# Kernel optimization log

Hardware: AMD Instinct MI355X
Metric: run time of the kernel (lower is better)

The kernel has to match this reference:

```python
import jax, jax.numpy as jnp
import numpy as np
from jax import lax

# Sizes
B, N, F = 8, 4096, 64          # clouds, points per cloud, feature dim
RATIO, RADIUS, K = 0.5, 0.2, 64  # fps ratio, ball radius, max_num_neighbors
S = int(N * RATIO)              # sampled centroids per cloud
H1, H2, H3 = 64, 64, 128        # MLP widths


def setup_inputs() -> dict:
    key = jax.random.key(0)
    ks = jax.random.split(key, 6)
    x = jax.random.normal(ks[0], (B * N, F), jnp.float32)
    pos = jax.random.uniform(ks[1], (B * N, 3), jnp.float32)  # unit cube
    batch = (jnp.arange(B * N) // N).astype(jnp.int32)  # equal-size clouds
    W1 = jax.random.normal(ks[2], (F + 3, H1), jnp.float32) * 0.1
    b1 = jnp.zeros((H1,), jnp.float32)
    W2 = jax.random.normal(ks[3], (H1, H2), jnp.float32) * 0.1
    b2 = jnp.zeros((H2,), jnp.float32)
    W3 = jax.random.normal(ks[4], (H2, H3), jnp.float32) * 0.1
    b3 = jnp.zeros((H3,), jnp.float32)
    return dict(x=x, pos=pos, batch=batch, W1=W1, b1=b1, W2=W2, b2=b2, W3=W3, b3=b3)


def fps_indices(pos_b):
    """Farthest point sampling for one cloud. pos_b: [N,3] -> [S] int32 indices."""
    def step(carry, _):
        cur, dmin = carry
        d = jnp.sum((pos_b - pos_b[cur]) ** 2, axis=-1)  # [N]
        dmin = jnp.minimum(dmin, d)
        nxt = jnp.argmax(dmin).astype(jnp.int32)
        return (nxt, dmin), cur
    init = (jnp.int32(0), jnp.full((N,), jnp.inf, jnp.float32))
    (_, _), sel = lax.scan(step, init, None, length=S)
    return sel


def reference(x, pos, batch, W1, b1, W2, b2, W3, b3):
    x3 = x.reshape(B, N, F)
    pos3 = pos.reshape(B, N, 3)
    batch3 = batch.reshape(B, N)

    # fps returns indices only -> no gradient path through sampling
    idx = jax.vmap(fps_indices)(lax.stop_gradient(pos3))  # [B,S]
    bi = jnp.arange(B)[:, None]
    pos_s = pos3[bi, idx]  # [B,S,3] sampled centroids

    # radius ball query: nearest-K within RADIUS (cap = max_num_neighbors)
    d2 = jnp.sum((pos_s[:, :, None, :] - pos3[:, None, :, :]) ** 2, axis=-1)  # [B,S,N]
    neg_d2, nbr = lax.top_k(-d2, K)          # [B,S,K] nearest K per centroid
    valid = (-neg_d2) <= RADIUS * RADIUS     # [B,S,K] inside-ball mask

    # PointNetConv: message = MLP(concat(x_j, pos_j - pos_i)), aggr = max
    gi = jnp.arange(B)[:, None, None]
    x_j = x3[gi, nbr]                          # [B,S,K,F]
    rel = pos3[gi, nbr] - pos_s[:, :, None, :]  # [B,S,K,3]
    h = jnp.concatenate([x_j, rel], axis=-1)    # [B,S,K,F+3]
    h = jax.nn.relu(h @ W1 + b1)
    h = jax.nn.relu(h @ W2 + b2)
    h = jax.nn.relu(h @ W3 + b3)                # [B,S,K,H3]
    h = jnp.where(valid[..., None], h, -jnp.inf)
    # each centroid is its own neighbor (dist 0 <= RADIUS), so max is finite
    out = jnp.max(h, axis=2)                    # [B,S,H3]

    x_out = out.reshape(B * S, H3)
    pos_out = pos_s.reshape(B * S, 3)
    batch_out = batch3[bi, idx].reshape(B * S)
    return x_out, pos_out, batch_out
```

## Files before the change

kernel.cpp:

```cpp
#include <hip/hip_runtime.h>
#include <cstdint>
#include <cstddef>

#define BB 8
#define NN 4096
#define FF 64
#define SS 2048
#define KK 64
#define H1c 64
#define H2c 64
#define H3c 128
#define R2 0.04f
#define CAP 448
#define NY1 240

typedef unsigned long long ull;
typedef __attribute__((ext_vector_type(4))) float f32x4;
typedef __attribute__((ext_vector_type(8))) short bf16x8;

__device__ __forceinline__ float d2_exact(float ax, float ay, float az,
                                          float bx, float by, float bz) {
  float dx = __fsub_rn(ax, bx);
  float dy = __fsub_rn(ay, by);
  float dz = __fsub_rn(az, bz);
  return __fadd_rn(__fadd_rn(__fmul_rn(dx, dx), __fmul_rn(dy, dy)), __fmul_rn(dz, dz));
}

__device__ __forceinline__ unsigned short f2bf(float f) {
  unsigned u = __float_as_uint(f);
  return (unsigned short)((u + 0x7fffu + ((u >> 16) & 1u)) >> 16);
}

#define WAVE_MAX_DPP(v)                                                        \
  do {                                                                         \
    v = max(v, __builtin_amdgcn_update_dpp(0, v, 0x111, 0xf, 0xf, true));      \
    v = max(v, __builtin_amdgcn_update_dpp(0, v, 0x112, 0xf, 0xf, true));      \
    v = max(v, __builtin_amdgcn_update_dpp(0, v, 0x114, 0xf, 0xf, true));      \
    v = max(v, __builtin_amdgcn_update_dpp(0, v, 0x118, 0xf, 0xf, true));      \
    v = max(v, __builtin_amdgcn_update_dpp(0, v, 0x142, 0xf, 0xf, true));      \
    v = max(v, __builtin_amdgcn_update_dpp(0, v, 0x143, 0xf, 0xf, true));      \
  } while (0)

__global__ __launch_bounds__(512) void fused_kernel(
    const float* __restrict__ pos, const float* __restrict__ x,
    const float* __restrict__ W1, const float* __restrict__ b1,
    const float* __restrict__ W2, const float* __restrict__ W3,
    float* __restrict__ pos_out, float* __restrict__ batch_out,
    unsigned short* __restrict__ y1b, unsigned short* __restrict__ w2p,
    unsigned short* __restrict__ w3p) {
  __shared__ __align__(16) char smem[49152];
  __shared__ ull skey[2][8];
  const int tid = threadIdx.x;

  if (blockIdx.x < BB) {
    float* plds = (float*)smem;
    const int b = blockIdx.x;
    const float4* src = (const float4*)(pos + (size_t)b * NN * 3);
    float4* dstl = (float4*)plds;
#pragma unroll
    for (int k = 0; k < 6; ++k) dstl[tid + k * 512] = src[tid + k * 512];
    __syncthreads();

    float px[8], py[8], pz[8], dmin[8];
#pragma unroll
    for (int i = 0; i < 8; ++i) {
      int p = tid * 8 + i;
      px[i] = plds[p * 3 + 0];
      py[i] = plds[p * 3 + 1];
      pz[i] = plds[p * 3 + 2];
      dmin[i] = INFINITY;
    }
    const int lane = tid & 63, wv = tid >> 6;
    float cx = plds[0], cy = plds[1], cz = plds[2];

    for (int s = 0; s < SS; ++s) {
      if (tid == 0) {
        int o = b * SS + s;
        pos_out[o * 3 + 0] = cx;
        pos_out[o * 3 + 1] = cy;
        pos_out[o * 3 + 2] = cz;
      }
#pragma unroll
      for (int i = 0; i < 8; ++i) {
        float d = d2_exact(px[i], py[i], pz[i], cx, cy, cz);
        dmin[i] = fminf(dmin[i], d);
      }
      float m0 = fmaxf(fmaxf(dmin[0], dmin[1]), fmaxf(dmin[2], dmin[3]));
      float m1 = fmaxf(fmaxf(dmin[4], dmin[5]), fmaxf(dmin[6], dmin[7]));
      const float lmax = fmaxf(m0, m1);
      int lidx = 0;
#pragma unroll
      for (int i = 7; i >= 0; --i)
        if (__float_as_int(dmin[i]) == __float_as_int(lmax)) lidx = i;

      const int lv = __float_as_int(lmax);
      int v = lv;
      WAVE_MAX_DPP(v);
      const int wmax = __builtin_amdgcn_readlane(v, 63);
      const ull bal = __ballot(lv == wmax);
      const int wl = (int)__builtin_ctzll(bal);
      const int wli = __builtin_amdgcn_readlane(lidx, wl);
      const int widx = ((wv << 6) + wl) * 8 + wli;
      const int buf = s & 1;
      if (lane == 0)
        skey[buf][wv] = ((ull)(unsigned)wmax << 32) | (unsigned)(~widx);
      __syncthreads();

      ull ka = skey[buf][0];
#pragma unroll
      for (int q = 1; q < 8; ++q) {
        ull kq = skey[buf][q];
        if (kq > ka) ka = kq;
      }
      const int cur = (int)(~(unsigned)(ka & 0xffffffffu));
      cx = plds[cur * 3 + 0];
      cy = plds[cur * 3 + 1];
      cz = plds[cur * 3 + 2];
    }
    for (int i = tid; i < SS; i += 512) batch_out[b * SS + i] = (float)b;
    return;
  }

  if (blockIdx.x == BB) {
    for (int e = tid; e < 4096; e += 512) {
      int j = e & 7, l = (e >> 3) & 63, s = (e >> 9) & 1, c = e >> 10;
      w2p[e] = f2bf(W2[(s * 32 + 8 * (l >> 4) + j) * H2c + c * 16 + (l & 15)]);
    }
    for (int e = tid; e < 8192; e += 512) {
      int j = e & 7, l = (e >> 3) & 63, s = (e >> 9) & 1, c = e >> 10;
      w3p[e] = f2bf(W3[(s * 32 + 8 * (l >> 4) + j) * H3c + c * 16 + (l & 15)]);
    }
    return;
  }

  float(*xs)[65] = (float(*)[65])smem;
  const int cid = blockIdx.x - BB - 1;
  for (int t = cid; t < 512; t += NY1) {
    const int r0 = t * 64;
    const float4* src = (const float4*)(x + (size_t)r0 * FF);
#pragma unroll
    for (int q = 0; q < 2; q++) {
      int p = tid + q * 512;
      float4 v = src[p];
      int row = (p * 4) >> 6, col = (p * 4) & 63;
      xs[row][col + 0] = v.x;
      xs[row][col + 1] = v.y;
      xs[row][col + 2] = v.z;
      xs[row][col + 3] = v.w;
    }
    __syncthreads();
    const int c4 = (tid & 15) * 4, kb = (tid >> 4) * 2;
    float acc[2][4];
#pragma unroll
    for (int kq = 0; kq < 2; kq++) {
      acc[kq][0] = b1[c4 + 0];
      acc[kq][1] = b1[c4 + 1];
      acc[kq][2] = b1[c4 + 2];
      acc[kq][3] = b1[c4 + 3];
    }
    for (int f = 0; f < FF; ++f) {
      float4 w = *(const float4*)(W1 + f * H1c + c4);
#pragma unroll
      for (int kq = 0; kq < 2; kq++) {
        float a = xs[kb + kq][f];
        acc[kq][0] += a * w.x;
        acc[kq][1] += a * w.y;
        acc[kq][2] += a * w.z;
        acc[kq][3] += a * w.w;
      }
    }
#pragma unroll
    for (int kq = 0; kq < 2; kq++) {
      ushort4 o;
      o.x = f2bf(acc[kq][0]);
      o.y = f2bf(acc[kq][1]);
      o.z = f2bf(acc[kq][2]);
      o.w = f2bf(acc[kq][3]);
      *(ushort4*)(y1b + (size_t)(r0 + kb + kq) * H1c + c4) = o;
    }
    __syncthreads();
  }
}

__global__ __launch_bounds__(256) void ballq_kernel(const float* __restrict__ pos,
                                                    const float* __restrict__ pos_out,
                                                    int* __restrict__ nbr) {
  __shared__ float plds[NN * 3];
  __shared__ __align__(16) ull kc[4][CAP];
  const int tid = threadIdx.x;
  const int b = blockIdx.x >> 6;
  const int chunk = blockIdx.x & 63;
  const float4* src = (const float4*)(pos + (size_t)b * NN * 3);
  float4* dstl = (float4*)plds;
#pragma unroll
  for (int k = 0; k < 12; k++) dstl[tid + k * 256] = src[tid + k * 256];
  __syncthreads();

  const int w = tid >> 6, lane = tid & 63;
  for (int t8 = 0; t8 < 8; ++t8) {
    const int s = chunk * 32 + w * 8 + t8;
    const int g = b * SS + s;
    const float cx = pos_out[g * 3 + 0], cy = pos_out[g * 3 + 1], cz = pos_out[g * 3 + 2];
    int cnt = 0;
    for (int t = 0; t < 64; ++t) {
      int j = t * 64 + lane;
      float d2 = d2_exact(plds[j * 3 + 0], plds[j * 3 + 1], plds[j * 3 + 2], cx, cy, cz);
      bool pred = (d2 <= R2);
      unsigned long long mask = __ballot(pred);
      if (pred) {
        int p = cnt + __popcll(mask & ((1ull << lane) - 1ull));
        if (p < CAP) kc[w][p] = ((ull)__float_as_uint(d2) << 32) | (unsigned)j;
      }
      cnt += (int)__popcll(mask);
    }
    int M = cnt < CAP ? cnt : CAP;
    __syncthreads();

    if (M <= 64) {
      int v = (lane < M) ? (b * NN + (int)(unsigned)(kc[w][lane] & 0xffffffffu)) : -1;
      nbr[(size_t)g * KK + lane] = v;
    } else {
      ull mk[7];
      int rk[7];
#pragma unroll
      for (int q = 0; q < 7; q++) {
        int p = lane + q * 64;
        mk[q] = (p < M) ? kc[w][p] : ~0ull;
        rk[q] = 0;
      }
      int i = 0;
      for (; i + 2 <= M; i += 2) {
        ull ka = kc[w][i], kb2 = kc[w][i + 1];
#pragma unroll
        for (int q = 0; q < 7; q++)
          rk[q] += (int)(ka < mk[q]) + (int)(kb2 < mk[q]);
      }
      if (i < M) {
        ull ka = kc[w][i];
#pragma unroll
        for (int q = 0; q < 7; q++) rk[q] += (int)(ka < mk[q]);
      }
#pragma unroll
      for (int q = 0; q < 7; q++) {
        int p = lane + q * 64;
        if (p < M && rk[q] < KK)
          nbr[(size_t)g * KK + rk[q]] = b * NN + (int)(unsigned)(mk[q] & 0xffffffffu);
      }
    }
    __syncthreads();
  }
}

__global__ __launch_bounds__(256) void mlp_kernel(
    const float* __restrict__ pos, const unsigned short* __restrict__ y1b,
    const float* __restrict__ W1, const float* __restrict__ b2,
    const float* __restrict__ b3, const unsigned short* __restrict__ w2p,
    const unsigned short* __restrict__ w3p, const int* __restrict__ nbr,
    const float* __restrict__ pos_out, float* __restrict__ x_out) {
  __shared__ __align__(16) unsigned short lw2[4096];
  __shared__ __align__(16) unsigned short lw3[8192];
  __shared__ float w1r[3][64];
  __shared__ int nl[64];
  __shared__ float red[4][128];
  __shared__ __align__(16) unsigned short h2t[4][16][88];
  const int tid = threadIdx.x;
  const int lane = tid & 63, wv = tid >> 6;
  const int lrow = lane & 15, g16 = lane >> 4;

  {
    const uint4* s2 = (const uint4*)w2p;
    uint4* d2v = (uint4*)lw2;
    for (int i = tid; i < 512; i += 256) d2v[i] = s2[i];
    const uint4* s3 = (const uint4*)w3p;
    uint4* d3v = (uint4*)lw3;
    for (int i = tid; i < 1024; i += 256) d3v[i] = s3[i];
    if (tid < 192) w1r[tid / 64][tid % 64] = W1[(64 + tid / 64) * H1c + (tid % 64)];
  }
  const bf16x8* w2f = (const bf16x8*)lw2;
  const bf16x8* w3f = (const bf16x8*)lw3;

  for (int pass = 0; pass < 4; ++pass) {
    const int g = blockIdx.x * 4 + pass;
    if (tid < 64) nl[tid] = nbr[(size_t)g * KK + tid];
    const float cx = pos_out[g * 3 + 0], cy = pos_out[g * 3 + 1],
                cz = pos_out[g * 3 + 2];
    __syncthreads();

    const int r = wv * 16 + lrow;
    const int j = nl[r];

    bf16x8 a0 = (bf16x8)0, a1 = (bf16x8)0;
    if (j >= 0) {
      const float rx = pos[j * 3 + 0] - cx;
      const float ry = pos[j * 3 + 1] - cy;
      const float rz = pos[j * 3 + 2] - cz;
      const unsigned short* yr = y1b + (size_t)j * H1c;
      uint4 vlo = *(const uint4*)(yr + 8 * g16);
      uint4 vhi = *(const uint4*)(yr + 32 + 8 * g16);
      const unsigned* plo = (const unsigned*)&vlo;
      const unsigned* phi = (const unsigned*)&vhi;
#pragma unroll
      for (int q = 0; q < 4; ++q) {
        unsigned u = plo[q];
        int k0 = 8 * g16 + 2 * q;
        float e0 = __uint_as_float(u << 16) + rx * w1r[0][k0] + ry * w1r[1][k0] +
                   rz * w1r[2][k0];
        float e1 = __uint_as_float(u & 0xffff0000u) + rx * w1r[0][k0 + 1] +
                   ry * w1r[1][k0 + 1] + rz * w1r[2][k0 + 1];
        a0[2 * q] = (short)f2bf(fmaxf(e0, 0.f));
        a0[2 * q + 1] = (short)f2bf(fmaxf(e1, 0.f));
        unsigned u2 = phi[q];
        int k1 = 32 + k0;
        float f0 = __uint_as_float(u2 << 16) + rx * w1r[0][k1] + ry * w1r[1][k1] +
                   rz * w1r[2][k1];
        float f1 = __uint_as_float(u2 & 0xffff0000u) + rx * w1r[0][k1 + 1] +
                   ry * w1r[1][k1 + 1] + rz * w1r[2][k1 + 1];
        a1[2 * q] = (short)f2bf(fmaxf(f0, 0.f));
        a1[2 * q + 1] = (short)f2bf(fmaxf(f1, 0.f));
      }
    }

#pragma unroll
    for (int c = 0; c < 4; ++c) {
      float bb = b2[c * 16 + lrow];
      f32x4 acc = {bb, bb, bb, bb};
      acc = __builtin_amdgcn_mfma_f32_16x16x32_bf16(a0, w2f[(c * 2 + 0) * 64 + lane], acc, 0, 0, 0);
      acc = __builtin_amdgcn_mfma_f32_16x16x32_bf16(a1, w2f[(c * 2 + 1) * 64 + lane], acc, 0, 0, 0);
#pragma unroll
      for (int t = 0; t < 4; ++t)
        h2t[wv][4 * g16 + t][c * 16 + lrow] = f2bf(fmaxf(acc[t], 0.f));
    }

    bf16x8 a20 = *(const bf16x8*)&h2t[wv][lrow][8 * g16];
    bf16x8 a21 = *(const bf16x8*)&h2t[wv][lrow][32 + 8 * g16];

    float vmax[8];
#pragma unroll
    for (int c = 0; c < 8; ++c) {
      float bb = b3[c * 16 + lrow];
      f32x4 acc = {bb, bb, bb, bb};
      acc = __builtin_amdgcn_mfma_f32_16x16x32_bf16(a20, w3f[(c * 2 + 0) * 64 + lane], acc, 0, 0, 0);
      acc = __builtin_amdgcn_mfma_f32_16x16x32_bf16(a21, w3f[(c * 2 + 1) * 64 + lane], acc, 0, 0, 0);
      float m = -INFINITY;
#pragma unroll
      for (int t = 0; t < 4; ++t) {
        int rg = wv * 16 + 4 * g16 + t;
        float val = (nl[rg] >= 0) ? fmaxf(acc[t], 0.f) : -INFINITY;
        m = fmaxf(m, val);
      }
      m = fmaxf(m, __shfl_xor(m, 16));
      m = fmaxf(m, __shfl_xor(m, 32));
      vmax[c] = m;
    }
    if (g16 == 0) {
#pragma unroll
      for (int c = 0; c < 8; ++c) red[wv][c * 16 + lrow] = vmax[c];
    }
    __syncthreads();
    if (tid < H3c) {
      float m = fmaxf(fmaxf(red[0][tid], red[1][tid]), fmaxf(red[2][tid], red[3][tid]));
      x_out[(size_t)g * H3c + tid] = m;
    }
  }
}

extern "C" void kernel_launch(void* const* d_in, const int* in_sizes, int n_in,
                              void* d_out, int out_size, void* d_ws, size_t ws_size,
                              hipStream_t stream) {
  const float* x = (const float*)d_in[0];
  const float* pos = (const float*)d_in[1];
  const float* W1 = (const float*)d_in[3];
  const float* b1 = (const float*)d_in[4];
  const float* W2 = (const float*)d_in[5];
  const float* b2 = (const float*)d_in[6];
  const float* W3 = (const float*)d_in[7];
  const float* b3 = (const float*)d_in[8];

  float* out = (float*)d_out;
  float* x_out = out;
  float* pos_out = out + (size_t)BB * SS * H3c;
  float* batch_out = pos_out + (size_t)BB * SS * 3;

  const size_t y1_bytes = (size_t)BB * NN * H1c * sizeof(unsigned short);
  const size_t nbr_bytes = (size_t)BB * SS * KK * sizeof(int);
  const size_t w2p_bytes = 4096 * sizeof(unsigned short);
  const size_t w3p_bytes = 8192 * sizeof(unsigned short);
  if (ws_size < y1_bytes + nbr_bytes + w2p_bytes + w3p_bytes) return;
  unsigned short* y1b = (unsigned short*)d_ws;
  int* nbr = (int*)((char*)d_ws + y1_bytes);
  unsigned short* w2p = (unsigned short*)((char*)d_ws + y1_bytes + nbr_bytes);
  unsigned short* w3p = w2p + 4096;

  fused_kernel<<<BB + 1 + NY1, 512, 0, stream>>>(pos, x, W1, b1, W2, W3,
                                                 pos_out, batch_out, y1b, w2p, w3p);
  ballq_kernel<<<BB * 64, 256, 0, stream>>>(pos, pos_out, nbr);
  mlp_kernel<<<BB * SS / 4, 256, 0, stream>>>(pos, y1b, W1, b2, b3, w2p, w3p,
                                              nbr, pos_out, x_out);
}
```

Measured before the change: 1.377 ms.

## Process two FPS clouds per block and carry winner coordinates through LDS

Each FPS block now handles two point clouds at once, interleaving their distance updates and reductions so that one barrier per step serves both clouds. The winning point's coordinates are published in shared memory with its key, which removes the dependent LDS lookup of the selected point, and points are loaded straight from global memory rather than staged in LDS. The intent is to amortise the per-step barrier and reduction latency of this serial 2048-step loop across two independent chains. The cost is doubled register use and ALU work per thread, which may lengthen each step.

```diff
diff --git a/kernel.cpp b/kernel.cpp
--- a/kernel.cpp
+++ b/kernel.cpp
@@ -12,6 +12,7 @@
 #define H3c 128
 #define R2 0.04f
 #define CAP 448
+#define NFPS 4
 #define NY1 240
 
 typedef unsigned long long ull;
@@ -48,80 +49,108 @@
     float* __restrict__ pos_out, float* __restrict__ batch_out,
     unsigned short* __restrict__ y1b, unsigned short* __restrict__ w2p,
     unsigned short* __restrict__ w3p) {
-  __shared__ __align__(16) char smem[49152];
-  __shared__ ull skey[2][8];
+  __shared__ float xs[64][65];
+  __shared__ ull skey[2][2][8];
+  __shared__ f32x4 scoord[2][2][8];
   const int tid = threadIdx.x;
 
-  if (blockIdx.x < BB) {
-    float* plds = (float*)smem;
-    const int b = blockIdx.x;
-    const float4* src = (const float4*)(pos + (size_t)b * NN * 3);
-    float4* dstl = (float4*)plds;
-#pragma unroll
-    for (int k = 0; k < 6; ++k) dstl[tid + k * 512] = src[tid + k * 512];
-    __syncthreads();
-
-    float px[8], py[8], pz[8], dmin[8];
-#pragma unroll
-    for (int i = 0; i < 8; ++i) {
-      int p = tid * 8 + i;
-      px[i] = plds[p * 3 + 0];
-      py[i] = plds[p * 3 + 1];
-      pz[i] = plds[p * 3 + 2];
-      dmin[i] = INFINITY;
-    }
+  if (blockIdx.x < NFPS) {
+    const int b0 = blockIdx.x * 2;
     const int lane = tid & 63, wv = tid >> 6;
-    float cx = plds[0], cy = plds[1], cz = plds[2];
+
+    float px[2][8], py[2][8], pz[2][8], dmin[2][8];
+    float cx[2], cy[2], cz[2];
+#pragma unroll
+    for (int c = 0; c < 2; ++c) {
+      const float* pb = pos + (size_t)(b0 + c) * (NN * 3) + (size_t)tid * 24;
+      float f[24];
+#pragma unroll
+      for (int q = 0; q < 6; ++q) {
+        float4 v = *(const float4*)(pb + 4 * q);
+        f[4 * q + 0] = v.x;
+        f[4 * q + 1] = v.y;
+        f[4 * q + 2] = v.z;
+        f[4 * q + 3] = v.w;
+      }
+#pragma unroll
+      for (int i = 0; i < 8; ++i) {
+        px[c][i] = f[3 * i + 0];
+        py[c][i] = f[3 * i + 1];
+        pz[c][i] = f[3 * i + 2];
+        dmin[c][i] = INFINITY;
+      }
+      cx[c] = pos[(size_t)(b0 + c) * (NN * 3) + 0];
+      cy[c] = pos[(size_t)(b0 + c) * (NN * 3) + 1];
+      cz[c] = pos[(size_t)(b0 + c) * (NN * 3) + 2];
+    }
 
     for (int s = 0; s < SS; ++s) {
       if (tid == 0) {
-        int o = b * SS + s;
-        pos_out[o * 3 + 0] = cx;
-        pos_out[o * 3 + 1] = cy;
-        pos_out[o * 3 + 2] = cz;
-      }
-#pragma unroll
-      for (int i = 0; i < 8; ++i) {
-        float d = d2_exact(px[i], py[i], pz[i], cx, cy, cz);
-        dmin[i] = fminf(dmin[i], d);
-      }
-      float m0 = fmaxf(fmaxf(dmin[0], dmin[1]), fmaxf(dmin[2], dmin[3]));
-      float m1 = fmaxf(fmaxf(dmin[4], dmin[5]), fmaxf(dmin[6], dmin[7]));
-      const float lmax = fmaxf(m0, m1);
-      int lidx = 0;
-#pragma unroll
-      for (int i = 7; i >= 0; --i)
-        if (__float_as_int(dmin[i]) == __float_as_int(lmax)) lidx = i;
-
-      const int lv = __float_as_int(lmax);
-      int v = lv;
-      WAVE_MAX_DPP(v);
-      const int wmax = __builtin_amdgcn_readlane(v, 63);
-      const ull bal = __ballot(lv == wmax);
-      const int wl = (int)__builtin_ctzll(bal);
-      const int wli = __builtin_amdgcn_readlane(lidx, wl);
-      const int widx = ((wv << 6) + wl) * 8 + wli;
+#pragma unroll
+        for (int c = 0; c < 2; ++c) {
+          int o = (b0 + c) * SS + s;
+          pos_out[o * 3 + 0] = cx[c];
+          pos_out[o * 3 + 1] = cy[c];
+          pos_out[o * 3 + 2] = cz[c];
+        }
+      }
       const int buf = s & 1;
-      if (lane == 0)
-        skey[buf][wv] = ((ull)(unsigned)wmax << 32) | (unsigned)(~widx);
+#pragma unroll
+      for (int c = 0; c < 2; ++c) {
+#pragma unroll
+        for (int i = 0; i < 8; ++i) {
+          float d = d2_exact(px[c][i], py[c][i], pz[c][i], cx[c], cy[c], cz[c]);
+          dmin[c][i] = fminf(dmin[c][i], d);
+        }
+        float m0 = fmaxf(fmaxf(dmin[c][0], dmin[c][1]), fmaxf(dmin[c][2], dmin[c][3]));
+        float m1 = fmaxf(fmaxf(dmin[c][4], dmin[c][5]), fmaxf(dmin[c][6], dmin[c][7]));
+        const float lmax = fmaxf(m0, m1);
+        int lidx = 0;
+        float sx = px[c][0], sy = py[c][0], sz = pz[c][0];
+#pragma unroll
+        for (int i = 7; i >= 1; --i) {
+          bool eq = (__float_as_int(dmin[c][i]) == __float_as_int(lmax));
+          lidx = eq ? i : lidx;
+          sx = eq ? px[c][i] : sx;
+          sy = eq ? py[c][i] : sy;
+          sz = eq ? pz[c][i] : sz;
+        }
+        const int lv = __float_as_int(lmax);
+        int v = lv;
+        WAVE_MAX_DPP(v);
+        const int wmax = __builtin_amdgcn_readlane(v, 63);
+        const ull bal = __ballot(lv == wmax);
+        const int wl = (int)__builtin_ctzll(bal);
+        if (lane == wl) {
+          const int gidx = tid * 8 + lidx;
+          skey[buf][c][wv] = ((ull)(unsigned)wmax << 32) | (unsigned)(~gidx);
+          scoord[buf][c][wv] = (f32x4){sx, sy, sz, 0.f};
+        }
+      }
       __syncthreads();
-
-      ull ka = skey[buf][0];
-#pragma unroll
-      for (int q = 1; q < 8; ++q) {
-        ull kq = skey[buf][q];
-        if (kq > ka) ka = kq;
-      }
-      const int cur = (int)(~(unsigned)(ka & 0xffffffffu));
-      cx = plds[cur * 3 + 0];
-      cy = plds[cur * 3 + 1];
-      cz = plds[cur * 3 + 2];
-    }
-    for (int i = tid; i < SS; i += 512) batch_out[b * SS + i] = (float)b;
+#pragma unroll
+      for (int c = 0; c < 2; ++c) {
+        ull bk = skey[buf][c][0];
+        f32x4 bc = scoord[buf][c][0];
+#pragma unroll
+        for (int q = 1; q < 8; ++q) {
+          ull kq = skey[buf][c][q];
+          f32x4 cq = scoord[buf][c][q];
+          if (kq > bk) { bk = kq; bc = cq; }
+        }
+        cx[c] = bc.x;
+        cy[c] = bc.y;
+        cz[c] = bc.z;
+      }
+    }
+    for (int i = tid; i < SS; i += 512) {
+      batch_out[(b0 + 0) * SS + i] = (float)(b0 + 0);
+      batch_out[(b0 + 1) * SS + i] = (float)(b0 + 1);
+    }
     return;
   }
 
-  if (blockIdx.x == BB) {
+  if (blockIdx.x == NFPS) {
     for (int e = tid; e < 4096; e += 512) {
       int j = e & 7, l = (e >> 3) & 63, s = (e >> 9) & 1, c = e >> 10;
       w2p[e] = f2bf(W2[(s * 32 + 8 * (l >> 4) + j) * H2c + c * 16 + (l & 15)]);
@@ -133,8 +162,7 @@
     return;
   }
 
-  float(*xs)[65] = (float(*)[65])smem;
-  const int cid = blockIdx.x - BB - 1;
+  const int cid = blockIdx.x - NFPS - 1;
   for (int t = cid; t < 512; t += NY1) {
     const int r0 = t * 64;
     const float4* src = (const float4*)(x + (size_t)r0 * FF);
@@ -391,8 +419,8 @@
   unsigned short* w2p = (unsigned short*)((char*)d_ws + y1_bytes + nbr_bytes);
   unsigned short* w3p = w2p + 4096;
 
-  fused_kernel<<<BB + 1 + NY1, 512, 0, stream>>>(pos, x, W1, b1, W2, W3,
-                                                 pos_out, batch_out, y1b, w2p, w3p);
+  fused_kernel<<<NFPS + 1 + NY1, 512, 0, stream>>>(pos, x, W1, b1, W2, W3,
+                                                   pos_out, batch_out, y1b, w2p, w3p);
   ballq_kernel<<<BB * 64, 256, 0, stream>>>(pos, pos_out, nbr);
   mlp_kernel<<<BB * SS / 4, 256, 0, stream>>>(pos, y1b, W1, b2, b3, w2p, w3p,
                                               nbr, pos_out, x_out);
```

After: 3.012 ms. +118.7%, slower.

## Fuse ball query into MLP kernel using planar position arrays

Applied to the files above, without the earlier changes.

Removes the separate ball-query kernel and the global neighbor-index buffer. Each MLP block now runs the radius search for its four centroids, one wave per centroid, and keeps the neighbor lists in shared memory. Point positions are read from structure-of-arrays planes written by the setup block, streamed as float4 from global memory instead of staged in LDS. This saves a launch and the nbr write/read round trip, but every block rescans all 4096 points of its cloud from global/L2. The extra kc array also raises LDS use and may lower occupancy.

```diff
diff --git a/kernel.cpp b/kernel.cpp
--- a/kernel.cpp
+++ b/kernel.cpp
@@ -47,7 +47,8 @@
     const float* __restrict__ W2, const float* __restrict__ W3,
     float* __restrict__ pos_out, float* __restrict__ batch_out,
     unsigned short* __restrict__ y1b, unsigned short* __restrict__ w2p,
-    unsigned short* __restrict__ w3p) {
+    unsigned short* __restrict__ w3p, float* __restrict__ xpln,
+    float* __restrict__ ypln, float* __restrict__ zpln) {
   __shared__ __align__(16) char smem[49152];
   __shared__ ull skey[2][8];
   const int tid = threadIdx.x;
@@ -130,6 +131,11 @@
       int j = e & 7, l = (e >> 3) & 63, s = (e >> 9) & 1, c = e >> 10;
       w3p[e] = f2bf(W3[(s * 32 + 8 * (l >> 4) + j) * H3c + c * 16 + (l & 15)]);
     }
+    for (int i = tid; i < BB * NN; i += 512) {
+      xpln[i] = pos[3 * i + 0];
+      ypln[i] = pos[3 * i + 1];
+      zpln[i] = pos[3 * i + 2];
+    }
     return;
   }
 
@@ -182,85 +188,18 @@
   }
 }
 
-__global__ __launch_bounds__(256) void ballq_kernel(const float* __restrict__ pos,
-                                                    const float* __restrict__ pos_out,
-                                                    int* __restrict__ nbr) {
-  __shared__ float plds[NN * 3];
-  __shared__ __align__(16) ull kc[4][CAP];
-  const int tid = threadIdx.x;
-  const int b = blockIdx.x >> 6;
-  const int chunk = blockIdx.x & 63;
-  const float4* src = (const float4*)(pos + (size_t)b * NN * 3);
-  float4* dstl = (float4*)plds;
-#pragma unroll
-  for (int k = 0; k < 12; k++) dstl[tid + k * 256] = src[tid + k * 256];
-  __syncthreads();
-
-  const int w = tid >> 6, lane = tid & 63;
-  for (int t8 = 0; t8 < 8; ++t8) {
-    const int s = chunk * 32 + w * 8 + t8;
-    const int g = b * SS + s;
-    const float cx = pos_out[g * 3 + 0], cy = pos_out[g * 3 + 1], cz = pos_out[g * 3 + 2];
-    int cnt = 0;
-    for (int t = 0; t < 64; ++t) {
-      int j = t * 64 + lane;
-      float d2 = d2_exact(plds[j * 3 + 0], plds[j * 3 + 1], plds[j * 3 + 2], cx, cy, cz);
-      bool pred = (d2 <= R2);
-      unsigned long long mask = __ballot(pred);
-      if (pred) {
-        int p = cnt + __popcll(mask & ((1ull << lane) - 1ull));
-        if (p < CAP) kc[w][p] = ((ull)__float_as_uint(d2) << 32) | (unsigned)j;
-      }
-      cnt += (int)__popcll(mask);
-    }
-    int M = cnt < CAP ? cnt : CAP;
-    __syncthreads();
-
-    if (M <= 64) {
-      int v = (lane < M) ? (b * NN + (int)(unsigned)(kc[w][lane] & 0xffffffffu)) : -1;
-      nbr[(size_t)g * KK + lane] = v;
-    } else {
-      ull mk[7];
-      int rk[7];
-#pragma unroll
-      for (int q = 0; q < 7; q++) {
-        int p = lane + q * 64;
-        mk[q] = (p < M) ? kc[w][p] : ~0ull;
-        rk[q] = 0;
-      }
-      int i = 0;
-      for (; i + 2 <= M; i += 2) {
-        ull ka = kc[w][i], kb2 = kc[w][i + 1];
-#pragma unroll
-        for (int q = 0; q < 7; q++)
-          rk[q] += (int)(ka < mk[q]) + (int)(kb2 < mk[q]);
-      }
-      if (i < M) {
-        ull ka = kc[w][i];
-#pragma unroll
-        for (int q = 0; q < 7; q++) rk[q] += (int)(ka < mk[q]);
-      }
-#pragma unroll
-      for (int q = 0; q < 7; q++) {
-        int p = lane + q * 64;
-        if (p < M && rk[q] < KK)
-          nbr[(size_t)g * KK + rk[q]] = b * NN + (int)(unsigned)(mk[q] & 0xffffffffu);
-      }
-    }
-    __syncthreads();
-  }
-}
-
-__global__ __launch_bounds__(256) void mlp_kernel(
-    const float* __restrict__ pos, const unsigned short* __restrict__ y1b,
-    const float* __restrict__ W1, const float* __restrict__ b2,
-    const float* __restrict__ b3, const unsigned short* __restrict__ w2p,
-    const unsigned short* __restrict__ w3p, const int* __restrict__ nbr,
+__global__ __launch_bounds__(256) void bqmlp_kernel(
+    const float* __restrict__ pos, const float* __restrict__ xpln,
+    const float* __restrict__ ypln, const float* __restrict__ zpln,
+    const unsigned short* __restrict__ y1b, const float* __restrict__ W1,
+    const float* __restrict__ b2, const float* __restrict__ b3,
+    const unsigned short* __restrict__ w2p, const unsigned short* __restrict__ w3p,
     const float* __restrict__ pos_out, float* __restrict__ x_out) {
   __shared__ __align__(16) unsigned short lw2[4096];
   __shared__ __align__(16) unsigned short lw3[8192];
   __shared__ float w1r[3][64];
-  __shared__ int nl[64];
+  __shared__ __align__(16) ull kc[4][CAP];
+  __shared__ int nbl[4][64];
   __shared__ float red[4][128];
   __shared__ __align__(16) unsigned short h2t[4][16][88];
   const int tid = threadIdx.x;
@@ -279,12 +218,104 @@
   const bf16x8* w2f = (const bf16x8*)lw2;
   const bf16x8* w3f = (const bf16x8*)lw3;
 
-  for (int pass = 0; pass < 4; ++pass) {
-    const int g = blockIdx.x * 4 + pass;
-    if (tid < 64) nl[tid] = nbr[(size_t)g * KK + tid];
+  const int g0 = blockIdx.x * 4;
+  const int b = blockIdx.x >> 9;
+  const float4* xp4 = (const float4*)(xpln + (size_t)b * NN);
+  const float4* yp4 = (const float4*)(ypln + (size_t)b * NN);
+  const float4* zp4 = (const float4*)(zpln + (size_t)b * NN);
+
+  {
+    const int g = g0 + wv;
     const float cx = pos_out[g * 3 + 0], cy = pos_out[g * 3 + 1],
                 cz = pos_out[g * 3 + 2];
-    __syncthreads();
+    const ull lt = (1ull << lane) - 1ull;
+    int cnt = 0;
+    for (int t = 0; t < 16; ++t) {
+      const int f4 = t * 64 + lane;
+      float4 xv = xp4[f4], yv = yp4[f4], zv = zp4[f4];
+      const int j0 = f4 * 4;
+      {
+        float d2 = d2_exact(xv.x, yv.x, zv.x, cx, cy, cz);
+        bool pred = (d2 <= R2);
+        ull mask = __ballot(pred);
+        if (pred) {
+          int p = cnt + (int)__popcll(mask & lt);
+          if (p < CAP) kc[wv][p] = ((ull)__float_as_uint(d2) << 32) | (unsigned)(j0 + 0);
+        }
+        cnt += (int)__popcll(mask);
+      }
+      {
+        float d2 = d2_exact(xv.y, yv.y, zv.y, cx, cy, cz);
+        bool pred = (d2 <= R2);
+        ull mask = __ballot(pred);
+        if (pred) {
+          int p = cnt + (int)__popcll(mask & lt);
+          if (p < CAP) kc[wv][p] = ((ull)__float_as_uint(d2) << 32) | (unsigned)(j0 + 1);
+        }
+        cnt += (int)__popcll(mask);
+      }
+      {
+        float d2 = d2_exact(xv.z, yv.z, zv.z, cx, cy, cz);
+        bool pred = (d2 <= R2);
+        ull mask = __ballot(pred);
+        if (pred) {
+          int p = cnt + (int)__popcll(mask & lt);
+          if (p < CAP) kc[wv][p] = ((ull)__float_as_uint(d2) << 32) | (unsigned)(j0 + 2);
+        }
+        cnt += (int)__popcll(mask);
+      }
+      {
+        float d2 = d2_exact(xv.w, yv.w, zv.w, cx, cy, cz);
+        bool pred = (d2 <= R2);
+        ull mask = __ballot(pred);
+        if (pred) {
+          int p = cnt + (int)__popcll(mask & lt);
+          if (p < CAP) kc[wv][p] = ((ull)__float_as_uint(d2) << 32) | (unsigned)(j0 + 3);
+        }
+        cnt += (int)__popcll(mask);
+      }
+    }
+    int M = cnt < CAP ? cnt : CAP;
+
+    if (M <= 64) {
+      nbl[wv][lane] =
+          (lane < M) ? (b * NN + (int)(unsigned)(kc[wv][lane] & 0xffffffffu)) : -1;
+    } else {
+      ull mk[7];
+      int rk[7];
+#pragma unroll
+      for (int q = 0; q < 7; q++) {
+        int p = lane + q * 64;
+        mk[q] = (p < M) ? kc[wv][p] : ~0ull;
+        rk[q] = 0;
+      }
+      int i = 0;
+      for (; i + 2 <= M; i += 2) {
+        ull ka = kc[wv][i], kb2 = kc[wv][i + 1];
+#pragma unroll
+        for (int q = 0; q < 7; q++)
+          rk[q] += (int)(ka < mk[q]) + (int)(kb2 < mk[q]);
+      }
+      if (i < M) {
+        ull ka = kc[wv][i];
+#pragma unroll
+        for (int q = 0; q < 7; q++) rk[q] += (int)(ka < mk[q]);
+      }
+#pragma unroll
+      for (int q = 0; q < 7; q++) {
+        int p = lane + q * 64;
+        if (p < M && rk[q] < KK)
+          nbl[wv][rk[q]] = b * NN + (int)(unsigned)(mk[q] & 0xffffffffu);
+      }
+    }
+  }
+  __syncthreads();
+
+  for (int pass = 0; pass < 4; ++pass) {
+    const int g = g0 + pass;
+    const float cx = pos_out[g * 3 + 0], cy = pos_out[g * 3 + 1],
+                cz = pos_out[g * 3 + 2];
+    const int* nl = nbl[pass];
 
     const int r = wv * 16 + lrow;
     const int j = nl[r];
@@ -361,6 +392,7 @@
       float m = fmaxf(fmaxf(red[0][tid], red[1][tid]), fmaxf(red[2][tid], red[3][tid]));
       x_out[(size_t)g * H3c + tid] = m;
     }
+    __syncthreads();
   }
 }
 
@@ -382,18 +414,20 @@
   float* batch_out = pos_out + (size_t)BB * SS * 3;
 
   const size_t y1_bytes = (size_t)BB * NN * H1c * sizeof(unsigned short);
-  const size_t nbr_bytes = (size_t)BB * SS * KK * sizeof(int);
   const size_t w2p_bytes = 4096 * sizeof(unsigned short);
   const size_t w3p_bytes = 8192 * sizeof(unsigned short);
-  if (ws_size < y1_bytes + nbr_bytes + w2p_bytes + w3p_bytes) return;
+  const size_t pln_bytes = (size_t)BB * NN * sizeof(float);
+  if (ws_size < y1_bytes + w2p_bytes + w3p_bytes + 3 * pln_bytes) return;
   unsigned short* y1b = (unsigned short*)d_ws;
-  int* nbr = (int*)((char*)d_ws + y1_bytes);
-  unsigned short* w2p = (unsigned short*)((char*)d_ws + y1_bytes + nbr_bytes);
+  unsigned short* w2p = (unsigned short*)((char*)d_ws + y1_bytes);
   unsigned short* w3p = w2p + 4096;
-
-  fused_kernel<<<BB + 1 + NY1, 512, 0, stream>>>(pos, x, W1, b1, W2, W3,
-                                                 pos_out, batch_out, y1b, w2p, w3p);
-  ballq_kernel<<<BB * 64, 256, 0, stream>>>(pos, pos_out, nbr);
-  mlp_kernel<<<BB * SS / 4, 256, 0, stream>>>(pos, y1b, W1, b2, b3, w2p, w3p,
-                                              nbr, pos_out, x_out);
+  float* xpln = (float*)((char*)d_ws + y1_bytes + w2p_bytes + w3p_bytes);
+  float* ypln = xpln + BB * NN;
+  float* zpln = ypln + BB * NN;
+
+  fused_kernel<<<BB + 1 + NY1, 512, 0, stream>>>(pos, x, W1, b1, W2, W3, pos_out,
+                                                 batch_out, y1b, w2p, w3p, xpln,
+                                                 ypln, zpln);
+  bqmlp_kernel<<<BB * SS / 4, 256, 0, stream>>>(pos, xpln, ypln, zpln, y1b, W1,
+                                                b2, b3, w2p, w3p, pos_out, x_out);
 }
```

Result: no change. 1.352 ms (-1.8%).
